# Performance work log

Measured on AMD Instinct MI355X. Metric: run time of the kernel, lower is better.

The kernel has to match this reference:

```python
import jax, jax.numpy as jnp
import numpy as np

B, S, IN_DIM, H, NC = 4, 512, 32, 64, 3

def setup_inputs() -> dict:
    key = jax.random.key(0)
    ks = jax.random.split(key, 20)
    def lin(k, i, o):
        bound = 1.0 / np.sqrt(i)
        kw, kb = jax.random.split(k)
        W = jax.random.uniform(kw, (i, o), jnp.float32, -bound, bound)
        b = jax.random.uniform(kb, (o,), jnp.float32, -bound, bound)
        return W, b
    W1, b1 = lin(ks[0], IN_DIM, H)
    W2, b2 = lin(ks[1], H, H)
    We1, be1 = lin(ks[2], 2 * H, H)
    We2, be2 = lin(ks[3], H, H)
    Wd1, bd1 = lin(ks[4], 2 * H, H // 2)
    Wd2, bd2 = lin(ks[5], H // 2, 1)
    Wc1, bc1 = lin(ks[6], 2 * H, 32)
    Wc2, bc2 = lin(ks[7], 32, NC)
    x = jax.random.normal(ks[8], (B, S, IN_DIM), jnp.float32)
    return {"x": x, "W1": W1, "b1": b1, "W2": W2, "b2": b2,
            "We1": We1, "be1": be1, "We2": We2, "be2": be2,
            "Wd1": Wd1, "bd1": bd1, "Wd2": Wd2, "bd2": bd2,
            "Wc1": Wc1, "bc1": bc1, "Wc2": Wc2, "bc2": bc2}

def reference(x, W1, b1, W2, b2, We1, be1, We2, be2,
              Wd1, bd1, Wd2, bd2, Wc1, bc1, Wc2, bc2):
    b, s, _ = x.shape
    # node encoder: Linear -> ReLU -> Linear
    nodes = jax.nn.relu(x @ W1 + b1) @ W2 + b2          # [b,s,H]
    h = nodes.shape[-1]
    # all-pairs concat: pairs[b,i,j] = [nodes[b,i], nodes[b,j]]
    pi = jnp.broadcast_to(nodes[:, :, None, :], (b, s, s, h))
    pj = jnp.broadcast_to(nodes[:, None, :, :], (b, s, s, h))
    pairs = jnp.concatenate([pi, pj], axis=-1)          # [b,s,s,2H]
    # edge network
    raw_msgs = jax.nn.relu(pairs @ We1 + be1) @ We2 + be2   # [b,s,s,H]
    # demon gate
    keep = jax.nn.sigmoid(jax.nn.relu(pairs @ Wd1 + bd1) @ Wd2 + bd2)  # [b,s,s,1]
    active = (raw_msgs * keep).sum(axis=2)              # [b,s,H]
    trash = (raw_msgs * (1.0 - keep)).sum(axis=2)       # [b,s,H]
    main_emb = (nodes + active).mean(axis=1)            # [b,H]
    trash_emb = trash.mean(axis=1)                      # [b,H]
    feat = jnp.concatenate([main_emb, trash_emb], axis=-1)  # [b,2H]
    return jax.nn.relu(feat @ Wc1 + bc1) @ Wc2 + bc2    # [b,NC]
```

## Files before the change

kernel.cpp:

```cpp
#include <hip/hip_runtime.h>

#define BB 4
#define SS 512
#define IND 32
#define HH 64
#define NCC 3

#define IPB 4
#define NPB (BB * 256)
#define NNB 512

#define OFF_U    0
#define OFF_V    (OFF_U + BB*SS*HH)
#define OFF_P    (OFF_V + BB*SS*HH)
#define OFF_QT   (OFF_P + BB*SS*32)
#define OFF_SN   (OFF_QT + 32*BB*SS)
#define OFF_SA   (OFF_SN + NNB*HH)
#define OFF_SH   (OFF_SA + NPB*HH)
#define OFF_SKP  (OFF_SH + NPB*HH)

__device__ __forceinline__ float rl(float v, int l) {
    return __uint_as_float(__builtin_amdgcn_readlane(__float_as_uint(v), l));
}

__global__ __launch_bounds__(256) void k_nodes(
    const float* __restrict__ x,  const float* __restrict__ W1, const float* __restrict__ b1,
    const float* __restrict__ W2, const float* __restrict__ b2,
    const float* __restrict__ We1,const float* __restrict__ be1,
    const float* __restrict__ Wd1,const float* __restrict__ bd1,
    float* __restrict__ ws)
{
    float* U = ws + OFF_U;  float* V4 = ws + OFF_V;
    float* P = ws + OFF_P;  float* Qt4 = ws + OFF_QT;
    float* SN = ws + OFF_SN;
    __shared__ float sn_lds[4][64];
    const int tid = threadIdx.x, wave = tid >> 6, lane = tid & 63;
    const int L = ((blockIdx.x & 7) << 6) | (blockIdx.x >> 3);
    const int node = L * 4 + wave;

    float xv = (lane < IND) ? x[node * IND + lane] : 0.0f;
    float h1 = b1[lane];
    #pragma unroll
    for (int k = 0; k < IND; k++)
        h1 = fmaf(__shfl(xv, k, 64), W1[k * HH + lane], h1);
    h1 = fmaxf(h1, 0.0f);

    float nd = b2[lane];
    #pragma unroll 16
    for (int k = 0; k < HH; k++)
        nd = fmaf(__shfl(h1, k, 64), W2[k * HH + lane], nd);

    float uv = be1[lane];
    float vv = 0.0f;
    float pq = (lane < 32) ? bd1[lane] : 0.0f;
    const float* WdCol = (lane < 32) ? (Wd1 + lane) : (Wd1 + HH * 32 + (lane - 32));
    #pragma unroll 16
    for (int k = 0; k < HH; k++) {
        float s = __shfl(nd, k, 64);
        uv = fmaf(s, We1[k * HH + lane], uv);
        vv = fmaf(s, We1[(HH + k) * HH + lane], vv);
        pq = fmaf(s, WdCol[k * 32], pq);
    }
    U[node * HH + lane] = uv;
    V4[(L * 64 + lane) * 4 + wave] = vv;
    if (lane < 32) {
        P[node * 32 + lane] = pq;
    } else {
        int k = lane - 32;
        Qt4[((k >> 2) * (BB * SS) + node) * 4 + (k & 3)] = pq;
    }

    sn_lds[wave][lane] = nd;
    __syncthreads();
    if (tid < 64)
        SN[L * 64 + tid] = (sn_lds[0][tid] + sn_lds[1][tid]) + (sn_lds[2][tid] + sn_lds[3][tid]);
}

__global__ __launch_bounds__(256, 3) void k_pairs(
    const float* __restrict__ wd2, const float* __restrict__ bd2,
    float* __restrict__ ws)
{
    const float*  U   = ws + OFF_U;
    const float4* V4  = (const float4*)(ws + OFF_V);
    const float*  P   = ws + OFF_P;
    const float4* Qt4 = (const float4*)(ws + OFF_QT);
    float* SA = ws + OFF_SA;  float* SHo = ws + OFF_SH;  float* SKp = ws + OFF_SKP;

    __shared__ float4 gs[4][64];
    __shared__ float redA[4][64], redH[4][64], redK[4];

    const int tid = threadIdx.x, wave = tid >> 6, lane = tid & 63;
    const int d   = blockIdx.x;
    const int xcd = d & 7;
    const int b   = xcd >> 1;
    const int jc  = xcd & 1;
    const int ic  = d >> 3;
    const int i0  = ic * IPB;
    const int lidx = (b << 8) | (ic << 1) | jc;
    const int jbase = b * SS + jc * 256 + wave * 64;

    const float u0 = U[(b * SS + i0 + 0) * HH + lane];
    const float u1 = U[(b * SS + i0 + 1) * HH + lane];
    const float u2 = U[(b * SS + i0 + 2) * HH + lane];
    const float u3 = U[(b * SS + i0 + 3) * HH + lane];
    const float pk0 = P[(b * SS + i0 + 0) * 32 + (lane & 31)];
    const float pk1 = P[(b * SS + i0 + 1) * 32 + (lane & 31)];
    const float pk2 = P[(b * SS + i0 + 2) * 32 + (lane & 31)];
    const float pk3 = P[(b * SS + i0 + 3) * 32 + (lane & 31)];
    const float wv  = wd2[lane & 31];
    const float bd2v = bd2[0];

    const float4* Qp = Qt4 + jbase + lane;
    const float4* Vp = V4 + (jbase >> 2) * 64 + lane;
    float4 q[8], v[16];
    #pragma unroll
    for (int kg = 0; kg < 8; kg++) q[kg] = Qp[kg * (BB * SS)];
    #pragma unroll
    for (int jq = 0; jq < 16; jq++) v[jq] = Vp[jq * 64];

    __builtin_amdgcn_sched_barrier(0);

    float a0 = bd2v, a1 = bd2v, a2 = bd2v, a3 = bd2v;
    #pragma unroll
    for (int kg = 0; kg < 8; kg++) {
        #pragma unroll
        for (int t = 0; t < 4; t++) {
            const int k = kg * 4 + t;
            float qv = (t == 0) ? q[kg].x : (t == 1) ? q[kg].y : (t == 2) ? q[kg].z : q[kg].w;
            float w  = rl(wv, k);
            a0 = fmaf(w, fmaxf(rl(pk0, k) + qv, 0.0f), a0);
            a1 = fmaf(w, fmaxf(rl(pk1, k) + qv, 0.0f), a1);
            a2 = fmaf(w, fmaxf(rl(pk2, k) + qv, 0.0f), a2);
            a3 = fmaf(w, fmaxf(rl(pk3, k) + qv, 0.0f), a3);
        }
    }
    float g0 = 1.0f / (1.0f + __expf(-a0));
    float g1 = 1.0f / (1.0f + __expf(-a1));
    float g2 = 1.0f / (1.0f + __expf(-a2));
    float g3 = 1.0f / (1.0f + __expf(-a3));
    float sk = (g0 + g1) + (g2 + g3);
    gs[wave][lane] = make_float4(g0, g1, g2, g3);
    __builtin_amdgcn_wave_barrier();

    float sa = 0.0f, sh = 0.0f;
    #pragma unroll
    for (int jq = 0; jq < 16; jq++) {
        #pragma unroll
        for (int t = 0; t < 4; t++) {
            float vv = (t == 0) ? v[jq].x : (t == 1) ? v[jq].y : (t == 2) ? v[jq].z : v[jq].w;
            float4 g4 = gs[wave][jq * 4 + t];
            float h0 = fmaxf(u0 + vv, 0.0f);
            float h1 = fmaxf(u1 + vv, 0.0f);
            float h2 = fmaxf(u2 + vv, 0.0f);
            float h3 = fmaxf(u3 + vv, 0.0f);
            sh += (h0 + h1) + (h2 + h3);
            sa = fmaf(g4.x, h0, sa);
            sa = fmaf(g4.y, h1, sa);
            sa = fmaf(g4.z, h2, sa);
            sa = fmaf(g4.w, h3, sa);
        }
    }

    redA[wave][lane] = sa;
    redH[wave][lane] = sh;
    #pragma unroll
    for (int off = 32; off; off >>= 1) sk += __shfl_xor(sk, off, 64);
    if (lane == 0) redK[wave] = sk;
    __syncthreads();

    if (tid < 64) {
        SA[lidx * 64 + tid]  = (redA[0][tid] + redA[1][tid]) + (redA[2][tid] + redA[3][tid]);
        SHo[lidx * 64 + tid] = (redH[0][tid] + redH[1][tid]) + (redH[2][tid] + redH[3][tid]);
        if (tid == 0)
            SKp[lidx * 16] = (redK[0] + redK[1]) + (redK[2] + redK[3]);
    }
}

__global__ __launch_bounds__(256) void k_final(
    const float* __restrict__ We2, const float* __restrict__ be2,
    const float* __restrict__ Wc1, const float* __restrict__ bc1,
    const float* __restrict__ Wc2, const float* __restrict__ bc2,
    const float* __restrict__ ws, float* __restrict__ out)
{
    const float4* SN4 = (const float4*)(ws + OFF_SN);
    const float4* SA4 = (const float4*)(ws + OFF_SA);
    const float4* SH4 = (const float4*)(ws + OFF_SH);
    const float*  SKp = ws + OFF_SKP;
    __shared__ float4 r4[3][16][16];
    __shared__ float redS[256], saL[64], shL[64];
    __shared__ float featL[128], c1L[32];
    const int tid = threadIdx.x, wave = tid >> 6, lane = tid & 63;
    const int grp = tid >> 4, l16 = tid & 15;
    const int b = blockIdx.x;

    float4 sn4 = make_float4(0.f, 0.f, 0.f, 0.f);
    float4 sa4 = sn4, sh4 = sn4;
    #pragma unroll
    for (int r = 0; r < 8; r++) {
        float4 t = SN4[(b * 128 + r * 16 + grp) * 16 + l16];
        sn4.x += t.x; sn4.y += t.y; sn4.z += t.z; sn4.w += t.w;
    }
    #pragma unroll
    for (int r = 0; r < 16; r++) {
        float4 t = SA4[(b * 256 + r * 16 + grp) * 16 + l16];
        float4 u = SH4[(b * 256 + r * 16 + grp) * 16 + l16];
        sa4.x += t.x; sa4.y += t.y; sa4.z += t.z; sa4.w += t.w;
        sh4.x += u.x; sh4.y += u.y; sh4.z += u.z; sh4.w += u.w;
    }
    r4[0][grp][l16] = sn4;  r4[1][grp][l16] = sa4;  r4[2][grp][l16] = sh4;
    redS[tid] = SKp[(b * 256 + tid) * 16];
    __syncthreads();

    if (wave == 0) {
        const int li = lane >> 2, comp = lane & 3;
        float snT = 0.f, saF = 0.f, shF = 0.f;
        #pragma unroll
        for (int g = 0; g < 16; g++) {
            snT += ((const float*)&r4[0][g][li])[comp];
            saF += ((const float*)&r4[1][g][li])[comp];
            shF += ((const float*)&r4[2][g][li])[comp];
        }
        float skp = (redS[lane] + redS[64 + lane]) + (redS[128 + lane] + redS[192 + lane]);
        #pragma unroll
        for (int off = 32; off; off >>= 1) skp += __shfl_xor(skp, off, 64);
        saL[lane] = saF;  shL[lane] = shF;

        float as = skp * be2[lane];
        float ts = (262144.0f - skp) * be2[lane];
        #pragma unroll 8
        for (int k = 0; k < HH; k++) {
            float w = We2[k * HH + lane];
            float sak = saL[k];
            as = fmaf(sak, w, as);
            ts = fmaf(shL[k] - sak, w, ts);
        }
        featL[lane]      = (snT + as) * (1.0f / 512.0f);
        featL[64 + lane] = ts * (1.0f / 512.0f);
    }
    __syncthreads();

    if (tid < 32) {
        float c1 = bc1[tid];
        #pragma unroll 8
        for (int k = 0; k < 128; k++)
            c1 = fmaf(featL[k], Wc1[k * 32 + tid], c1);
        c1L[tid] = fmaxf(c1, 0.0f);
    }
    __syncthreads();
    if (tid < NCC) {
        float o = bc2[tid];
        #pragma unroll
        for (int k = 0; k < 32; k++)
            o = fmaf(c1L[k], Wc2[k * NCC + tid], o);
        out[b * NCC + tid] = o;
    }
}

extern "C" void kernel_launch(void* const* d_in, const int* in_sizes, int n_in,
                              void* d_out, int out_size, void* d_ws, size_t ws_size,
                              hipStream_t stream) {
    const float* x   = (const float*)d_in[0];
    const float* W1  = (const float*)d_in[1];
    const float* b1  = (const float*)d_in[2];
    const float* W2  = (const float*)d_in[3];
    const float* b2  = (const float*)d_in[4];
    const float* We1 = (const float*)d_in[5];
    const float* be1 = (const float*)d_in[6];
    const float* We2 = (const float*)d_in[7];
    const float* be2 = (const float*)d_in[8];
    const float* Wd1 = (const float*)d_in[9];
    const float* bd1 = (const float*)d_in[10];
    const float* wd2 = (const float*)d_in[11];
    const float* bd2 = (const float*)d_in[12];
    const float* Wc1 = (const float*)d_in[13];
    const float* bc1 = (const float*)d_in[14];
    const float* Wc2 = (const float*)d_in[15];
    const float* bc2 = (const float*)d_in[16];
    float* ws  = (float*)d_ws;
    float* out = (float*)d_out;

    k_nodes<<<dim3(NNB), dim3(256), 0, stream>>>(x, W1, b1, W2, b2, We1, be1, Wd1, bd1, ws);
    k_pairs<<<dim3(NPB), dim3(256), 0, stream>>>(wd2, bd2, ws);
    k_final<<<dim3(BB), dim3(256), 0, stream>>>(We2, be2, Wc1, bc1, Wc2, bc2, ws, out);
}
```

Baseline: 33.77 us.

## Share j-tile Q and V across four i-groups via LDS in 1024-thread blocks

Merges four former blocks into one 1024-thread block that processes 16 i rows for the same j half. The Q and V tiles are loaded cooperatively into dynamic LDS once and reused by all four sub-groups, which removes redundant global loads and the per-wave register-held q/v arrays. In exchange it uses about 120 KB of LDS per block, allows only one block per CU, and adds a block-wide barrier plus LDS reads inside the inner loops.

```diff
diff --git a/kernel.cpp b/kernel.cpp
--- a/kernel.cpp
+++ b/kernel.cpp
@@ -6,8 +6,7 @@
 #define HH 64
 #define NCC 3
 
-#define IPB 4
-#define NPB (BB * 256)
+#define NPB 256
 #define NNB 512
 
 #define OFF_U    0
@@ -16,8 +15,16 @@
 #define OFF_QT   (OFF_P + BB*SS*32)
 #define OFF_SN   (OFF_QT + 32*BB*SS)
 #define OFF_SA   (OFF_SN + NNB*HH)
-#define OFF_SH   (OFF_SA + NPB*HH)
-#define OFF_SKP  (OFF_SH + NPB*HH)
+#define OFF_SH   (OFF_SA + 1024*HH)
+#define OFF_SKP  (OFF_SH + 1024*HH)
+
+#define L_QT   0
+#define L_V    8192
+#define L_GS   24576
+#define L_RA   28672
+#define L_RH   29696
+#define L_RK   30720
+#define L_TOT  30736
 
 __device__ __forceinline__ float rl(float v, int l) {
     return __uint_as_float(__builtin_amdgcn_readlane(__float_as_uint(v), l));
@@ -76,28 +83,43 @@
         SN[L * 64 + tid] = (sn_lds[0][tid] + sn_lds[1][tid]) + (sn_lds[2][tid] + sn_lds[3][tid]);
 }
 
-__global__ __launch_bounds__(256, 3) void k_pairs(
+__global__ __launch_bounds__(1024, 1) void k_pairs(
     const float* __restrict__ wd2, const float* __restrict__ bd2,
     float* __restrict__ ws)
 {
+    extern __shared__ float smem[];
+    float4* QtL = (float4*)(smem + L_QT);
+    float4* VL  = (float4*)(smem + L_V);
+    float4* gs  = (float4*)(smem + L_GS);
+    float*  redA = smem + L_RA;
+    float*  redH = smem + L_RH;
+    float*  redK = smem + L_RK;
+
     const float*  U   = ws + OFF_U;
     const float4* V4  = (const float4*)(ws + OFF_V);
     const float*  P   = ws + OFF_P;
     const float4* Qt4 = (const float4*)(ws + OFF_QT);
     float* SA = ws + OFF_SA;  float* SHo = ws + OFF_SH;  float* SKp = ws + OFF_SKP;
 
-    __shared__ float4 gs[4][64];
-    __shared__ float redA[4][64], redH[4][64], redK[4];
-
-    const int tid = threadIdx.x, wave = tid >> 6, lane = tid & 63;
+    const int tid = threadIdx.x, w = tid >> 6, lane = tid & 63;
+    const int sub = w >> 2, wslot = w & 3;
     const int d   = blockIdx.x;
     const int xcd = d & 7;
     const int b   = xcd >> 1;
     const int jc  = xcd & 1;
     const int ic  = d >> 3;
-    const int i0  = ic * IPB;
-    const int lidx = (b << 8) | (ic << 1) | jc;
-    const int jbase = b * SS + jc * 256 + wave * 64;
+    const int i0  = ic * 16 + sub * 4;
+    const int lidx = (b << 8) | (((ic << 2) | sub) << 1) | jc;
+    const int jb_blk = b * SS + jc * 256;
+
+    const int q0 = tid * 2, q1 = tid * 2 + 1;
+    float4 sq0 = Qt4[(q0 >> 8) * (BB * SS) + jb_blk + (q0 & 255)];
+    float4 sq1 = Qt4[(q1 >> 8) * (BB * SS) + jb_blk + (q1 & 255)];
+    const int vbase = (jb_blk >> 2) * 64;
+    float4 sv0 = V4[vbase + tid * 4 + 0];
+    float4 sv1 = V4[vbase + tid * 4 + 1];
+    float4 sv2 = V4[vbase + tid * 4 + 2];
+    float4 sv3 = V4[vbase + tid * 4 + 3];
 
     const float u0 = U[(b * SS + i0 + 0) * HH + lane];
     const float u1 = U[(b * SS + i0 + 1) * HH + lane];
@@ -110,28 +132,24 @@
     const float wv  = wd2[lane & 31];
     const float bd2v = bd2[0];
 
-    const float4* Qp = Qt4 + jbase + lane;
-    const float4* Vp = V4 + (jbase >> 2) * 64 + lane;
-    float4 q[8], v[16];
-    #pragma unroll
-    for (int kg = 0; kg < 8; kg++) q[kg] = Qp[kg * (BB * SS)];
-    #pragma unroll
-    for (int jq = 0; jq < 16; jq++) v[jq] = Vp[jq * 64];
-
-    __builtin_amdgcn_sched_barrier(0);
+    QtL[q0] = sq0;  QtL[q1] = sq1;
+    VL[tid * 4 + 0] = sv0;  VL[tid * 4 + 1] = sv1;
+    VL[tid * 4 + 2] = sv2;  VL[tid * 4 + 3] = sv3;
+    __syncthreads();
 
     float a0 = bd2v, a1 = bd2v, a2 = bd2v, a3 = bd2v;
     #pragma unroll
     for (int kg = 0; kg < 8; kg++) {
+        float4 q4 = QtL[kg * 256 + wslot * 64 + lane];
         #pragma unroll
         for (int t = 0; t < 4; t++) {
             const int k = kg * 4 + t;
-            float qv = (t == 0) ? q[kg].x : (t == 1) ? q[kg].y : (t == 2) ? q[kg].z : q[kg].w;
-            float w  = rl(wv, k);
-            a0 = fmaf(w, fmaxf(rl(pk0, k) + qv, 0.0f), a0);
-            a1 = fmaf(w, fmaxf(rl(pk1, k) + qv, 0.0f), a1);
-            a2 = fmaf(w, fmaxf(rl(pk2, k) + qv, 0.0f), a2);
-            a3 = fmaf(w, fmaxf(rl(pk3, k) + qv, 0.0f), a3);
+            float qv = (t == 0) ? q4.x : (t == 1) ? q4.y : (t == 2) ? q4.z : q4.w;
+            float ww = rl(wv, k);
+            a0 = fmaf(ww, fmaxf(rl(pk0, k) + qv, 0.0f), a0);
+            a1 = fmaf(ww, fmaxf(rl(pk1, k) + qv, 0.0f), a1);
+            a2 = fmaf(ww, fmaxf(rl(pk2, k) + qv, 0.0f), a2);
+            a3 = fmaf(ww, fmaxf(rl(pk3, k) + qv, 0.0f), a3);
         }
     }
     float g0 = 1.0f / (1.0f + __expf(-a0));
@@ -139,16 +157,17 @@
     float g2 = 1.0f / (1.0f + __expf(-a2));
     float g3 = 1.0f / (1.0f + __expf(-a3));
     float sk = (g0 + g1) + (g2 + g3);
-    gs[wave][lane] = make_float4(g0, g1, g2, g3);
+    gs[w * 64 + lane] = make_float4(g0, g1, g2, g3);
     __builtin_amdgcn_wave_barrier();
 
     float sa = 0.0f, sh = 0.0f;
     #pragma unroll
     for (int jq = 0; jq < 16; jq++) {
+        float4 v4 = VL[wslot * 1024 + jq * 64 + lane];
         #pragma unroll
         for (int t = 0; t < 4; t++) {
-            float vv = (t == 0) ? v[jq].x : (t == 1) ? v[jq].y : (t == 2) ? v[jq].z : v[jq].w;
-            float4 g4 = gs[wave][jq * 4 + t];
+            float vv = (t == 0) ? v4.x : (t == 1) ? v4.y : (t == 2) ? v4.z : v4.w;
+            float4 g4 = gs[w * 64 + jq * 4 + t];
             float h0 = fmaxf(u0 + vv, 0.0f);
             float h1 = fmaxf(u1 + vv, 0.0f);
             float h2 = fmaxf(u2 + vv, 0.0f);
@@ -161,18 +180,21 @@
         }
     }
 
-    redA[wave][lane] = sa;
-    redH[wave][lane] = sh;
+    redA[w * 64 + lane] = sa;
+    redH[w * 64 + lane] = sh;
     #pragma unroll
     for (int off = 32; off; off >>= 1) sk += __shfl_xor(sk, off, 64);
-    if (lane == 0) redK[wave] = sk;
-    __syncthreads();
-
-    if (tid < 64) {
-        SA[lidx * 64 + tid]  = (redA[0][tid] + redA[1][tid]) + (redA[2][tid] + redA[3][tid]);
-        SHo[lidx * 64 + tid] = (redH[0][tid] + redH[1][tid]) + (redH[2][tid] + redH[3][tid]);
-        if (tid == 0)
-            SKp[lidx * 16] = (redK[0] + redK[1]) + (redK[2] + redK[3]);
+    if (lane == 0) redK[w] = sk;
+    __syncthreads();
+
+    if (wslot == 0) {
+        const int base = sub * 4;
+        SA[lidx * 64 + lane]  = (redA[(base + 0) * 64 + lane] + redA[(base + 1) * 64 + lane])
+                              + (redA[(base + 2) * 64 + lane] + redA[(base + 3) * 64 + lane]);
+        SHo[lidx * 64 + lane] = (redH[(base + 0) * 64 + lane] + redH[(base + 1) * 64 + lane])
+                              + (redH[(base + 2) * 64 + lane] + redH[(base + 3) * 64 + lane]);
+        if (lane == 0)
+            SKp[lidx * 16] = (redK[base + 0] + redK[base + 1]) + (redK[base + 2] + redK[base + 3]);
     }
 }
 
@@ -279,7 +301,10 @@
     float* ws  = (float*)d_ws;
     float* out = (float*)d_out;
 
+    hipFuncSetAttribute((const void*)k_pairs,
+                        hipFuncAttributeMaxDynamicSharedMemorySize, L_TOT * 4);
+
     k_nodes<<<dim3(NNB), dim3(256), 0, stream>>>(x, W1, b1, W2, b2, We1, be1, Wd1, bd1, ws);
-    k_pairs<<<dim3(NPB), dim3(256), 0, stream>>>(wd2, bd2, ws);
+    k_pairs<<<dim3(NPB), dim3(1024), L_TOT * 4, stream>>>(wd2, bd2, ws);
     k_final<<<dim3(BB), dim3(256), 0, stream>>>(We2, be2, Wc1, bc1, Wc2, bc2, ws, out);
 }
```

Measured after the change: 34.63 us. +2.6%, slower.
